# Kernel tuning notes

Measured on AMD Instinct MI355X. Metric: run time of the kernel, lower is better.

## Reference

```python
import jax, jax.numpy as jnp
import numpy as np

H = 16  # n_heads

def setup_inputs() -> dict:
    key = jax.random.key(0)
    ks = jax.random.split(key, 11)
    B, L, D = 2, 2048, 1024
    w = 1.0 / np.sqrt(D).astype(np.float32)
    return {
        "query": jax.random.normal(ks[0], (B, L, D), jnp.float32),
        "key":   jax.random.normal(ks[1], (B, L, D), jnp.float32),
        "value": jax.random.normal(ks[2], (B, L, D), jnp.float32),
        "Wq": jax.random.normal(ks[3], (D, D), jnp.float32) * w,
        "bq": jax.random.normal(ks[4], (D,), jnp.float32) * 0.01,
        "Wk": jax.random.normal(ks[5], (D, D), jnp.float32) * w,
        "bk": jax.random.normal(ks[6], (D,), jnp.float32) * 0.01,
        "Wv": jax.random.normal(ks[7], (D, D), jnp.float32) * w,
        "bv": jax.random.normal(ks[8], (D,), jnp.float32) * 0.01,
        "Wo": jax.random.normal(ks[9], (D, D), jnp.float32) * w,
        "bo": jax.random.normal(ks[10], (D,), jnp.float32) * 0.01,
        "masksize": 256,
    }

def reference(query, key, value, Wq, bq, Wk, bk, Wv, bv, Wo, bo, masksize):
    B, L, D = query.shape
    d_k = D // H
    scale = 1.0 / np.sqrt(d_k).astype(np.float32)

    def proj(x, W, b):
        # nn.Linear: x @ W.T + b, then [B,L,H,d_k] -> [B,H,L,d_k]
        return (x @ W.T + b).reshape(B, L, H, d_k).transpose(0, 2, 1, 3)

    q = proj(query, Wq, bq)
    k = proj(key, Wk, bk)
    v = proj(value, Wv, bv)

    # Sliding-window float mask (faithful to original: a 0/1 FLOAT tensor is
    # passed as attn_mask to SDPA, so it is ADDED to scores, not -inf-masked).
    half = masksize // 2
    i = jnp.arange(L)[:, None]
    j = jnp.arange(L)[None, :]
    band = (jnp.abs(i - j) <= half).astype(q.dtype)  # [L, L]

    scores = jnp.einsum('bhqd,bhkd->bhqk', q, k) * scale + band  # [B,H,L,L]
    attn = jax.nn.softmax(scores, axis=-1)
    out = jnp.einsum('bhqk,bhkd->bhqd', attn, v)  # [B,H,L,d_k]
    out = out.transpose(0, 2, 1, 3).reshape(B, L, D)
    return out @ Wo.T + bo
```

## Files before the change

### kernel.cpp

```cpp
#include <hip/hip_runtime.h>
#include <hip/hip_bf16.h>

#define Hh 16
#define Ll 2048
#define Dd 1024
#define DK 64
#define Mm 4096
#define Kk 1024
#define Nn 1024

typedef short bf16x8 __attribute__((ext_vector_type(8)));
typedef float f32x4 __attribute__((ext_vector_type(4)));

static __device__ __forceinline__ unsigned short f2bf(float f) {
    union { __hip_bfloat16 b; unsigned short u; } cv;
    cv.b = __float2bfloat16(f);
    return cv.u;
}

static __device__ __forceinline__ unsigned packtr(float a, float b) {
    return __builtin_amdgcn_perm(__builtin_bit_cast(unsigned, b),
                                 __builtin_bit_cast(unsigned, a), 0x07060302u);
}

static __device__ __forceinline__ float fexp2(float x) {
    return __builtin_amdgcn_exp2f(x);
}

static __device__ __forceinline__ void glds16(const ushort* g, ushort* l) {
    __builtin_amdgcn_global_load_lds((const __attribute__((address_space(1))) unsigned int*)g,
                                     (__attribute__((address_space(3))) unsigned int*)l,
                                     16, 0, 0);
}

__global__ __launch_bounds__(256) void cast_all(
    const float* __restrict__ q, const float* __restrict__ k, const float* __restrict__ v,
    const float* __restrict__ wq, const float* __restrict__ wk, const float* __restrict__ wv,
    const float* __restrict__ wo,
    ushort* __restrict__ qb, ushort* __restrict__ kb, ushort* __restrict__ vb,
    ushort* __restrict__ wqb, ushort* __restrict__ wkb, ushort* __restrict__ wvb,
    ushort* __restrict__ wob) {
    const int bx = blockIdx.x;
    const float4* s; ushort4* d; int base;
    if      (bx <  4096) { s = (const float4*)q;  d = (ushort4*)qb;  base = 0; }
    else if (bx <  8192) { s = (const float4*)k;  d = (ushort4*)kb;  base = 4096; }
    else if (bx < 12288) { s = (const float4*)v;  d = (ushort4*)vb;  base = 8192; }
    else if (bx < 13312) { s = (const float4*)wq; d = (ushort4*)wqb; base = 12288; }
    else if (bx < 14336) { s = (const float4*)wk; d = (ushort4*)wkb; base = 13312; }
    else if (bx < 15360) { s = (const float4*)wv; d = (ushort4*)wvb; base = 14336; }
    else                 { s = (const float4*)wo; d = (ushort4*)wob; base = 15360; }
    const int i = (bx - base) * 256 + threadIdx.x;
    float4 vv = s[i];
    ushort4 o;
    o.x = f2bf(vv.x); o.y = f2bf(vv.y); o.z = f2bf(vv.z); o.w = f2bf(vv.w);
    d[i] = o;
}

__global__ __launch_bounds__(256) void gemm_qkv(
    const ushort* __restrict__ A0, const ushort* __restrict__ A1, const ushort* __restrict__ A2,
    const ushort* __restrict__ W0, const ushort* __restrict__ W1, const ushort* __restrict__ W2,
    const float* __restrict__ b0, const float* __restrict__ b1, const float* __restrict__ b2,
    ushort* __restrict__ O0, ushort* __restrict__ O1, ushort* __restrict__ OVt) {
    __shared__ __align__(16) ushort SM[2 * 128 * 32];
    ushort* As = SM;
    ushort* Bs = SM + 4096;

    const int fl = blockIdx.x;
    const int xcd = fl & 7, bcoli = (fl >> 3) & 7, slot = fl >> 6;
    const int g = slot * 8 + xcd;
    const int z = g >> 5;
    const int browi = g & 31;

    const ushort* A = (z == 0) ? A0 : (z == 1) ? A1 : A2;
    const ushort* W = (z == 0) ? W0 : (z == 1) ? W1 : W2;
    const float* bias = (z == 0) ? b0 : (z == 1) ? b1 : b2;

    const int t = threadIdx.x;
    const int wave = t >> 6, lane = t & 63;
    const int quad = lane >> 4, l15 = lane & 15;
    const int brow = browi * 128, bcol = bcoli * 128;
    const int wr = (wave >> 1) * 64, wc = (wave & 1) * 64;
    const int gr = wave * 16 + (lane >> 2);
    const int gc = (lane & 3) * 8;

    f32x4 acc[4][4] = {};

    for (int k0 = 0; k0 < Kk; k0 += 32) {
        __syncthreads();
        glds16(A + (size_t)(brow + gr) * Kk + k0 + gc,      As + wave * 512);
        glds16(A + (size_t)(brow + 64 + gr) * Kk + k0 + gc, As + 2048 + wave * 512);
        glds16(W + (size_t)(bcol + gr) * Kk + k0 + gc,      Bs + wave * 512);
        glds16(W + (size_t)(bcol + 64 + gr) * Kk + k0 + gc, Bs + 2048 + wave * 512);
        __syncthreads();

        bf16x8 af[4], bfr[4];
#pragma unroll
        for (int i = 0; i < 4; i++)
            af[i] = *(const bf16x8*)(As + (wr + i * 16 + l15) * 32 + quad * 8);
#pragma unroll
        for (int j = 0; j < 4; j++)
            bfr[j] = *(const bf16x8*)(Bs + (wc + j * 16 + l15) * 32 + quad * 8);
#pragma unroll
        for (int i = 0; i < 4; i++)
#pragma unroll
            for (int j = 0; j < 4; j++)
                acc[i][j] = __builtin_amdgcn_mfma_f32_16x16x32_bf16(af[i], bfr[j], acc[i][j], 0, 0, 0);
    }

    if (z < 2) {
        ushort* Out = (z == 0) ? O0 : O1;
        const float oscl = (z == 0) ? 0.18033688f : 1.0f;
        const int b = brow >> 11;
        const int lbase = (brow & 2047) + wr;
        const int h = (bcol + wc) >> 6;
        ushort* T = SM + wave * 1280;
        __syncthreads();
#pragma unroll
        for (int i = 0; i < 4; i++) {
#pragma unroll
            for (int j = 0; j < 4; j++) {
                const float bv = bias[bcol + wc + j * 16 + l15];
#pragma unroll
                for (int r = 0; r < 4; r++)
                    T[(quad * 4 + r) * 80 + j * 16 + l15] = f2bf((acc[i][j][r] + bv) * oscl);
            }
            const int r8 = lane >> 3, c8 = lane & 7;
#pragma unroll
            for (int pass = 0; pass < 2; pass++) {
                const uint4 val = *(const uint4*)(T + (pass * 8 + r8) * 80 + c8 * 8);
                const int l = lbase + i * 16 + pass * 8 + r8;
                *(uint4*)(Out + ((size_t)(b * Hh + h) * Ll + l) * DK + c8 * 8) = val;
            }
        }
    } else {
        ushort* T = SM;
        const int b = brow >> 11;
        const int lbase = brow & 2047;
        const int npr = (wave & 1) * 16 + l15;
#pragma unroll
        for (int j = 0; j < 4; j++) {
            __syncthreads();
            const float bv = bias[bcol + wc + j * 16 + l15];
#pragma unroll
            for (int i = 0; i < 4; i++)
#pragma unroll
                for (int r = 0; r < 4; r++) {
                    const int m = wr + i * 16 + quad * 4 + r;
                    T[npr * 136 + m] = f2bf(acc[i][j][r] + bv);
                }
            __syncthreads();
#pragma unroll
            for (int cc = 0; cc < 2; cc++) {
                const int idx = t + cc * 256;
                const int ni = idx >> 4;
                const int ms = idx & 15;
                const int n = bcol + (ni >> 4) * 64 + j * 16 + (ni & 15);
                const int hh = n >> 6, dk = n & 63;
                uint4 val = *(const uint4*)(T + ni * 136 + ms * 8);
                *(uint4*)(OVt + ((size_t)(b * Hh + hh) * DK + dk) * Ll + lbase + ms * 8) = val;
            }
        }
    }
}

__global__ __launch_bounds__(256) void attn_kernel(const ushort* __restrict__ Q,
                                                   const ushort* __restrict__ Kp,
                                                   const ushort* __restrict__ Vt,
                                                   ushort* __restrict__ Oout,
                                                   const int* __restrict__ masksize) {
    __shared__ __align__(16) ushort Ks[2 * 128 * 32];
    __shared__ __align__(16) ushort Vs[64 * 128];
    const int t = threadIdx.x;
    const int wave = t >> 6, lane = t & 63;
    const int quad = lane >> 4, l15 = lane & 15;
    const int bx = blockIdx.x;
    const int bh = bx & 31, qc = bx >> 5;
    const int q0w = qc * 128 + wave * 32;
    const int half = masksize[0] >> 1;
    const unsigned wid = (unsigned)(2 * half);

    const ushort* Qb = Q + (size_t)bh * (Ll * DK);
    const ushort* Kb = Kp + (size_t)bh * (Ll * DK);
    const ushort* Vb = Vt + (size_t)bh * (DK * Ll);

    const bf16x8 qA0 = *(const bf16x8*)(Qb + (size_t)(q0w + l15) * DK + quad * 8);
    const bf16x8 qA1 = *(const bf16x8*)(Qb + (size_t)(q0w + l15) * DK + 32 + quad * 8);
    const bf16x8 qB0 = *(const bf16x8*)(Qb + (size_t)(q0w + 16 + l15) * DK + quad * 8);
    const bf16x8 qB1 = *(const bf16x8*)(Qb + (size_t)(q0w + 16 + l15) * DK + 32 + quad * 8);

    const float C2IN  = (1.0f - 24.0f) * 1.44269504088896f;
    const float C2OUT = -24.0f * 1.44269504088896f;
    const float E1 = 2.718281828f;

    bf16x8 onesf;
#pragma unroll
    for (int j = 0; j < 8; j++) onesf[j] = (short)0x3F80;

    f32x4 OA[4] = {}, OB[4] = {};
    f32x4 SA = {}, SB = {};

    const int krow = lane >> 2;
    const int kcol8 = (lane & 3) * 8;
    const int vdl = lane >> 4;
    const int vg0 = 2 * (lane & 15);

    for (int kt = 0; kt < Ll; kt += 128) {
        __syncthreads();
        if (wave < 2) {
            const int cbase = wave * 4;
#pragma unroll
            for (int c = 0; c < 4; c++)
#pragma unroll
                for (int pan = 0; pan < 2; pan++)
                    glds16(Kb + (size_t)(kt + (cbase + c) * 16 + krow) * DK + pan * 32 + kcol8,
                           Ks + (pan * 128 + (cbase + c) * 16) * 32);
        } else {
            const int sb = (wave - 2) * 8;
#pragma unroll
            for (int i = 0; i < 8; i++) {
                const int sidx = sb + i;
                const int d = sidx * 4 + vdl;
                const int g0 = vg0 ^ (d & 30);
                glds16(Vb + (size_t)d * Ll + kt + g0 * 4, Vs + sidx * 512);
            }
        }
        __syncthreads();

        const int qlo = q0w, qhi = q0w + 31;
        const bool allout = (kt + 127 < qlo - half) || (kt > qhi + half);
        const bool allin  = (kt >= qhi - half) && (kt + 127 <= qlo + half);
        const bool uniform = allin || allout;
        const float cinit = allin ? C2IN : C2OUT;
        f32x4 cvec = {cinit, cinit, cinit, cinit};

#pragma unroll
        for (int s = 0; s < 4; s++) {
            const bf16x8 kf00 = *(const bf16x8*)(Ks + ((2 * s) * 16 + l15) * 32 + quad * 8);
            const bf16x8 kf01 = *(const bf16x8*)(Ks + 4096 + ((2 * s) * 16 + l15) * 32 + quad * 8);
            const bf16x8 kf10 = *(const bf16x8*)(Ks + ((2 * s + 1) * 16 + l15) * 32 + quad * 8);
            const bf16x8 kf11 = *(const bf16x8*)(Ks + 4096 + ((2 * s + 1) * 16 + l15) * 32 + quad * 8);
            f32x4 zA0 = __builtin_amdgcn_mfma_f32_16x16x32_bf16(kf00, qA0, cvec, 0, 0, 0);
            zA0 = __builtin_amdgcn_mfma_f32_16x16x32_bf16(kf01, qA1, zA0, 0, 0, 0);
            f32x4 zA1 = __builtin_amdgcn_mfma_f32_16x16x32_bf16(kf10, qA0, cvec, 0, 0, 0);
            zA1 = __builtin_amdgcn_mfma_f32_16x16x32_bf16(kf11, qA1, zA1, 0, 0, 0);
            f32x4 zB0 = __builtin_amdgcn_mfma_f32_16x16x32_bf16(kf00, qB0, cvec, 0, 0, 0);
            zB0 = __builtin_amdgcn_mfma_f32_16x16x32_bf16(kf01, qB1, zB0, 0, 0, 0);
            f32x4 zB1 = __builtin_amdgcn_mfma_f32_16x16x32_bf16(kf10, qB0, cvec, 0, 0, 0);
            zB1 = __builtin_amdgcn_mfma_f32_16x16x32_bf16(kf11, qB1, zB1, 0, 0, 0);

            float pA[8], pB[8];
            if (uniform) {
#pragma unroll
                for (int g = 0; g < 2; g++)
#pragma unroll
                    for (int r = 0; r < 4; r++) {
                        pA[g * 4 + r] = fexp2(g ? zA1[r] : zA0[r]);
                        pB[g * 4 + r] = fexp2(g ? zB1[r] : zB0[r]);
                    }
            } else {
                const int kb = kt + s * 32 + quad * 4 + half;
#pragma unroll
                for (int g = 0; g < 2; g++)
#pragma unroll
                    for (int r = 0; r < 4; r++) {
                        const unsigned ttA = (unsigned)(kb + g * 16 + r - (q0w + l15));
                        const unsigned ttB = (unsigned)(kb + g * 16 + r - (q0w + 16 + l15));
                        pA[g * 4 + r] = fexp2(g ? zA1[r] : zA0[r]) * (ttA <= wid ? E1 : 1.0f);
                        pB[g * 4 + r] = fexp2(g ? zB1[r] : zB0[r]) * (ttB <= wid ? E1 : 1.0f);
                    }
            }

            bf16x8 pfA, pfB;
            ((unsigned*)&pfA)[0] = packtr(pA[0], pA[1]);
            ((unsigned*)&pfA)[1] = packtr(pA[2], pA[3]);
            ((unsigned*)&pfA)[2] = packtr(pA[4], pA[5]);
            ((unsigned*)&pfA)[3] = packtr(pA[6], pA[7]);
            ((unsigned*)&pfB)[0] = packtr(pB[0], pB[1]);
            ((unsigned*)&pfB)[1] = packtr(pB[2], pB[3]);
            ((unsigned*)&pfB)[2] = packtr(pB[4], pB[5]);
            ((unsigned*)&pfB)[3] = packtr(pB[6], pB[7]);

            SA = __builtin_amdgcn_mfma_f32_16x16x32_bf16(pfA, onesf, SA, 0, 0, 0);
            SB = __builtin_amdgcn_mfma_f32_16x16x32_bf16(pfB, onesf, SB, 0, 0, 0);

#pragma unroll
            for (int i = 0; i < 4; i++) {
                const int d = i * 16 + l15;
                const int x4 = (d & 30) * 4;
                const int bi = d * 128;
                const ushort4 v1 = *(const ushort4*)(Vs + bi + (((s * 8 + quad) * 4) ^ x4));
                const ushort4 v2 = *(const ushort4*)(Vs + bi + (((s * 8 + 4 + quad) * 4) ^ x4));
                bf16x8 vc;
                *(ushort4*)&vc = v1;
                *((ushort4*)&vc + 1) = v2;
                OA[i] = __builtin_amdgcn_mfma_f32_16x16x32_bf16(pfA, vc, OA[i], 0, 0, 0);
                OB[i] = __builtin_amdgcn_mfma_f32_16x16x32_bf16(pfB, vc, OB[i], 0, 0, 0);
            }
        }
    }

    float liA[4], liB[4];
#pragma unroll
    for (int r = 0; r < 4; r++) {
        liA[r] = 1.0f / SA[r];
        liB[r] = 1.0f / SB[r];
    }

    const int b = bh >> 4, h = bh & 15;
#pragma unroll
    for (int i = 0; i < 4; i++)
#pragma unroll
        for (int r = 0; r < 4; r++) {
            const int qa = q0w + quad * 4 + r;
            Oout[((size_t)b * Ll + qa) * Dd + h * DK + i * 16 + l15] = f2bf(OA[i][r] * liA[r]);
            Oout[((size_t)b * Ll + qa + 16) * Dd + h * DK + i * 16 + l15] = f2bf(OB[i][r] * liB[r]);
        }
}

__global__ __launch_bounds__(256) void gemm_o(const ushort* __restrict__ A,
                                              const ushort* __restrict__ W,
                                              const float* __restrict__ bias,
                                              float* __restrict__ Out) {
    __shared__ __align__(16) ushort As[64 * 32];
    __shared__ __align__(16) ushort Bs[128 * 32];
    const int fl = blockIdx.x;
    const int xcd = fl & 7, bcoli = (fl >> 3) & 7, slot = fl >> 6;
    const int g = slot * 8 + xcd;
    const int t = threadIdx.x;
    const int wave = t >> 6, lane = t & 63;
    const int quad = lane >> 4, l15 = lane & 15;
    const int brow = g * 64, bcol = bcoli * 128;
    const int wr = (wave >> 1) * 32, wc = (wave & 1) * 64;
    const int gr = wave * 16 + (lane >> 2);
    const int gc = (lane & 3) * 8;

    f32x4 acc[2][4] = {};

    for (int k0 = 0; k0 < Kk; k0 += 32) {
        __syncthreads();
        glds16(A + (size_t)(brow + gr) * Kk + k0 + gc,      As + wave * 512);
        glds16(W + (size_t)(bcol + gr) * Kk + k0 + gc,      Bs + wave * 512);
        glds16(W + (size_t)(bcol + 64 + gr) * Kk + k0 + gc, Bs + 2048 + wave * 512);
        __syncthreads();

        bf16x8 af[2], bfr[4];
#pragma unroll
        for (int i = 0; i < 2; i++)
            af[i] = *(const bf16x8*)(As + (wr + i * 16 + l15) * 32 + quad * 8);
#pragma unroll
        for (int j = 0; j < 4; j++)
            bfr[j] = *(const bf16x8*)(Bs + (wc + j * 16 + l15) * 32 + quad * 8);
#pragma unroll
        for (int i = 0; i < 2; i++)
#pragma unroll
            for (int j = 0; j < 4; j++)
                acc[i][j] = __builtin_amdgcn_mfma_f32_16x16x32_bf16(af[i], bfr[j], acc[i][j], 0, 0, 0);
    }

#pragma unroll
    for (int i = 0; i < 2; i++)
#pragma unroll
        for (int j = 0; j < 4; j++) {
            const int n = bcol + wc + j * 16 + l15;
            const float bv = bias[n];
#pragma unroll
            for (int r = 0; r < 4; r++) {
                const int m = brow + wr + i * 16 + quad * 4 + r;
                Out[(size_t)m * Nn + n] = acc[i][j][r] + bv;
            }
        }
}

extern "C" void kernel_launch(void* const* d_in, const int* in_sizes, int n_in,
                              void* d_out, int out_size, void* d_ws, size_t ws_size,
                              hipStream_t stream) {
    const float* query = (const float*)d_in[0];
    const float* key   = (const float*)d_in[1];
    const float* value = (const float*)d_in[2];
    const float* Wq = (const float*)d_in[3];
    const float* bq = (const float*)d_in[4];
    const float* Wk = (const float*)d_in[5];
    const float* bk = (const float*)d_in[6];
    const float* Wv = (const float*)d_in[7];
    const float* bv = (const float*)d_in[8];
    const float* Wo = (const float*)d_in[9];
    const float* bo = (const float*)d_in[10];
    const int* masksize = (const int*)d_in[11];

    char* ws = (char*)d_ws;
    const size_t MB = 1024 * 1024;
    ushort* qb  = (ushort*)(ws + 0 * MB);
    ushort* kbf = (ushort*)(ws + 8 * MB);
    ushort* vbf = (ushort*)(ws + 16 * MB);
    ushort* wqb = (ushort*)(ws + 24 * MB);
    ushort* wkb = (ushort*)(ws + 26 * MB);
    ushort* wvb = (ushort*)(ws + 28 * MB);
    ushort* wob = (ushort*)(ws + 30 * MB);
    ushort* Qp  = (ushort*)(ws + 32 * MB);
    ushort* Kp  = (ushort*)(ws + 40 * MB);
    ushort* Vt  = (ushort*)(ws + 48 * MB);
    ushort* AO  = (ushort*)(ws + 56 * MB);

    cast_all<<<16384, 256, 0, stream>>>(query, key, value, Wq, Wk, Wv, Wo,
                                        qb, kbf, vbf, wqb, wkb, wvb, wob);

    gemm_qkv<<<768, 256, 0, stream>>>(qb, kbf, vbf,
                                      wqb, wkb, wvb,
                                      bq, bk, bv,
                                      Qp, Kp, Vt);

    attn_kernel<<<512, 256, 0, stream>>>(Qp, Kp, Vt, AO, masksize);

    gemm_o<<<512, 256, 0, stream>>>(AO, wob, bo, (float*)d_out);
}
```

Baseline: 217.9 us.

## Split attention block into eight waves of sixteen query rows each

```diff
diff --git a/kernel.cpp b/kernel.cpp
--- a/kernel.cpp
+++ b/kernel.cpp
@@ -163,11 +163,11 @@
     }
 }
 
-__global__ __launch_bounds__(256) void attn_kernel(const ushort* __restrict__ Q,
-                                                   const ushort* __restrict__ Kp,
-                                                   const ushort* __restrict__ Vt,
-                                                   ushort* __restrict__ Oout,
-                                                   const int* __restrict__ masksize) {
+__global__ __launch_bounds__(512, 4) void attn_kernel(const ushort* __restrict__ Q,
+                                                      const ushort* __restrict__ Kp,
+                                                      const ushort* __restrict__ Vt,
+                                                      ushort* __restrict__ Oout,
+                                                      const int* __restrict__ masksize) {
     __shared__ __align__(16) ushort Ks[2 * 128 * 32];
     __shared__ __align__(16) ushort Vs[64 * 128];
     const int t = threadIdx.x;
@@ -175,7 +175,7 @@
     const int quad = lane >> 4, l15 = lane & 15;
     const int bx = blockIdx.x;
     const int bh = bx & 31, qc = bx >> 5;
-    const int q0w = qc * 128 + wave * 32;
+    const int q0w = qc * 128 + wave * 16;
     const int half = masksize[0] >> 1;
     const unsigned wid = (unsigned)(2 * half);
 
@@ -185,8 +185,6 @@
 
     const bf16x8 qA0 = *(const bf16x8*)(Qb + (size_t)(q0w + l15) * DK + quad * 8);
     const bf16x8 qA1 = *(const bf16x8*)(Qb + (size_t)(q0w + l15) * DK + 32 + quad * 8);
-    const bf16x8 qB0 = *(const bf16x8*)(Qb + (size_t)(q0w + 16 + l15) * DK + quad * 8);
-    const bf16x8 qB1 = *(const bf16x8*)(Qb + (size_t)(q0w + 16 + l15) * DK + 32 + quad * 8);
 
     const float C2IN  = (1.0f - 24.0f) * 1.44269504088896f;
     const float C2OUT = -24.0f * 1.44269504088896f;
@@ -196,8 +194,8 @@
 #pragma unroll
     for (int j = 0; j < 8; j++) onesf[j] = (short)0x3F80;
 
-    f32x4 OA[4] = {}, OB[4] = {};
-    f32x4 SA = {}, SB = {};
+    f32x4 OA[4] = {};
+    f32x4 SA = {};
 
     const int krow = lane >> 2;
     const int kcol8 = (lane & 3) * 8;
@@ -206,18 +204,18 @@
 
     for (int kt = 0; kt < Ll; kt += 128) {
         __syncthreads();
-        if (wave < 2) {
-            const int cbase = wave * 4;
-#pragma unroll
-            for (int c = 0; c < 4; c++)
+        if (wave < 4) {
+            const int cbase = wave * 2;
+#pragma unroll
+            for (int c = 0; c < 2; c++)
 #pragma unroll
                 for (int pan = 0; pan < 2; pan++)
                     glds16(Kb + (size_t)(kt + (cbase + c) * 16 + krow) * DK + pan * 32 + kcol8,
                            Ks + (pan * 128 + (cbase + c) * 16) * 32);
         } else {
-            const int sb = (wave - 2) * 8;
-#pragma unroll
-            for (int i = 0; i < 8; i++) {
+            const int sb = (wave - 4) * 4;
+#pragma unroll
+            for (int i = 0; i < 4; i++) {
                 const int sidx = sb + i;
                 const int d = sidx * 4 + vdl;
                 const int g0 = vg0 ^ (d & 30);
@@ -226,7 +224,7 @@
         }
         __syncthreads();
 
-        const int qlo = q0w, qhi = q0w + 31;
+        const int qlo = q0w, qhi = q0w + 15;
         const bool allout = (kt + 127 < qlo - half) || (kt > qhi + half);
         const bool allin  = (kt >= qhi - half) && (kt + 127 <= qlo + half);
         const bool uniform = allin || allout;
@@ -243,20 +241,14 @@
             zA0 = __builtin_amdgcn_mfma_f32_16x16x32_bf16(kf01, qA1, zA0, 0, 0, 0);
             f32x4 zA1 = __builtin_amdgcn_mfma_f32_16x16x32_bf16(kf10, qA0, cvec, 0, 0, 0);
             zA1 = __builtin_amdgcn_mfma_f32_16x16x32_bf16(kf11, qA1, zA1, 0, 0, 0);
-            f32x4 zB0 = __builtin_amdgcn_mfma_f32_16x16x32_bf16(kf00, qB0, cvec, 0, 0, 0);
-            zB0 = __builtin_amdgcn_mfma_f32_16x16x32_bf16(kf01, qB1, zB0, 0, 0, 0);
-            f32x4 zB1 = __builtin_amdgcn_mfma_f32_16x16x32_bf16(kf10, qB0, cvec, 0, 0, 0);
-            zB1 = __builtin_amdgcn_mfma_f32_16x16x32_bf16(kf11, qB1, zB1, 0, 0, 0);
-
-            float pA[8], pB[8];
+
+            float pA[8];
             if (uniform) {
 #pragma unroll
                 for (int g = 0; g < 2; g++)
 #pragma unroll
-                    for (int r = 0; r < 4; r++) {
+                    for (int r = 0; r < 4; r++)
                         pA[g * 4 + r] = fexp2(g ? zA1[r] : zA0[r]);
-                        pB[g * 4 + r] = fexp2(g ? zB1[r] : zB0[r]);
-                    }
             } else {
                 const int kb = kt + s * 32 + quad * 4 + half;
 #pragma unroll
@@ -264,24 +256,17 @@
 #pragma unroll
                     for (int r = 0; r < 4; r++) {
                         const unsigned ttA = (unsigned)(kb + g * 16 + r - (q0w + l15));
-                        const unsigned ttB = (unsigned)(kb + g * 16 + r - (q0w + 16 + l15));
                         pA[g * 4 + r] = fexp2(g ? zA1[r] : zA0[r]) * (ttA <= wid ? E1 : 1.0f);
-                        pB[g * 4 + r] = fexp2(g ? zB1[r] : zB0[r]) * (ttB <= wid ? E1 : 1.0f);
                     }
             }
 
-            bf16x8 pfA, pfB;
+            bf16x8 pfA;
             ((unsigned*)&pfA)[0] = packtr(pA[0], pA[1]);
             ((unsigned*)&pfA)[1] = packtr(pA[2], pA[3]);
             ((unsigned*)&pfA)[2] = packtr(pA[4], pA[5]);
             ((unsigned*)&pfA)[3] = packtr(pA[6], pA[7]);
-            ((unsigned*)&pfB)[0] = packtr(pB[0], pB[1]);
-            ((unsigned*)&pfB)[1] = packtr(pB[2], pB[3]);
-            ((unsigned*)&pfB)[2] = packtr(pB[4], pB[5]);
-            ((unsigned*)&pfB)[3] = packtr(pB[6], pB[7]);
 
             SA = __builtin_amdgcn_mfma_f32_16x16x32_bf16(pfA, onesf, SA, 0, 0, 0);
-            SB = __builtin_amdgcn_mfma_f32_16x16x32_bf16(pfB, onesf, SB, 0, 0, 0);
 
 #pragma unroll
             for (int i = 0; i < 4; i++) {
@@ -294,17 +279,13 @@
                 *(ushort4*)&vc = v1;
                 *((ushort4*)&vc + 1) = v2;
                 OA[i] = __builtin_amdgcn_mfma_f32_16x16x32_bf16(pfA, vc, OA[i], 0, 0, 0);
-                OB[i] = __builtin_amdgcn_mfma_f32_16x16x32_bf16(pfB, vc, OB[i], 0, 0, 0);
             }
         }
     }
 
-    float liA[4], liB[4];
-#pragma unroll
-    for (int r = 0; r < 4; r++) {
-        liA[r] = 1.0f / SA[r];
-        liB[r] = 1.0f / SB[r];
-    }
+    float liA[4];
+#pragma unroll
+    for (int r = 0; r < 4; r++) liA[r] = 1.0f / SA[r];
 
     const int b = bh >> 4, h = bh & 15;
 #pragma unroll
@@ -313,7 +294,6 @@
         for (int r = 0; r < 4; r++) {
             const int qa = q0w + quad * 4 + r;
             Oout[((size_t)b * Ll + qa) * Dd + h * DK + i * 16 + l15] = f2bf(OA[i][r] * liA[r]);
-            Oout[((size_t)b * Ll + qa + 16) * Dd + h * DK + i * 16 + l15] = f2bf(OB[i][r] * liB[r]);
         }
 }
 
@@ -409,7 +389,7 @@
                                       bq, bk, bv,
                                       Qp, Kp, Vt);
 
-    attn_kernel<<<512, 256, 0, stream>>>(Qp, Kp, Vt, AO, masksize);
+    attn_kernel<<<512, 512, 0, stream>>>(Qp, Kp, Vt, AO, masksize);
 
     gemm_o<<<512, 256, 0, stream>>>(AO, wob, bo, (float*)d_out);
 }
```

After: 220.5 us. About the same (+1.2%).

## Split attention key range across two wave groups and swizzle K LDS layout

Applied to the files above, without the earlier changes.

```diff
diff --git a/kernel.cpp b/kernel.cpp
--- a/kernel.cpp
+++ b/kernel.cpp
@@ -163,21 +163,24 @@
     }
 }
 
-__global__ __launch_bounds__(256) void attn_kernel(const ushort* __restrict__ Q,
-                                                   const ushort* __restrict__ Kp,
-                                                   const ushort* __restrict__ Vt,
-                                                   ushort* __restrict__ Oout,
-                                                   const int* __restrict__ masksize) {
-    __shared__ __align__(16) ushort Ks[2 * 128 * 32];
-    __shared__ __align__(16) ushort Vs[64 * 128];
+__global__ __launch_bounds__(512, 4) void attn_kernel(const ushort* __restrict__ Q,
+                                                      const ushort* __restrict__ Kp,
+                                                      const ushort* __restrict__ Vt,
+                                                      ushort* __restrict__ Oout,
+                                                      const int* __restrict__ masksize) {
+    __shared__ __align__(16) ushort SM[4 * 8192];
     const int t = threadIdx.x;
     const int wave = t >> 6, lane = t & 63;
     const int quad = lane >> 4, l15 = lane & 15;
     const int bx = blockIdx.x;
     const int bh = bx & 31, qc = bx >> 5;
-    const int q0w = qc * 128 + wave * 32;
+    const int p = wave & 3, h = wave >> 2;
+    const int q0w = qc * 128 + p * 32;
     const int half = masksize[0] >> 1;
     const unsigned wid = (unsigned)(2 * half);
+
+    ushort* KsH = SM + h * 8192;
+    ushort* VsH = SM + 16384 + h * 8192;
 
     const ushort* Qb = Q + (size_t)bh * (Ll * DK);
     const ushort* Kb = Kp + (size_t)bh * (Ll * DK);
@@ -200,28 +203,32 @@
     f32x4 SA = {}, SB = {};
 
     const int krow = lane >> 2;
-    const int kcol8 = (lane & 3) * 8;
+    const int kcol8 = (((lane & 3) ^ ((lane >> 3) & 3)) * 8);
+    const int qsw8 = (quad ^ ((l15 >> 1) & 3)) * 8;
     const int vdl = lane >> 4;
     const int vg0 = 2 * (lane & 15);
 
-    for (int kt = 0; kt < Ll; kt += 128) {
-        __syncthreads();
-        if (wave < 2) {
-            const int cbase = wave * 4;
-#pragma unroll
-            for (int c = 0; c < 4; c++)
+    for (int it = 0; it < 8; ++it) {
+        const int kt = h * 1024 + it * 128;
+        __syncthreads();
+        if ((wave & 2) == 0) {
+            const int a = wave & 1;
+#pragma unroll
+            for (int c = 0; c < 4; c++) {
+                const int cidx = a * 4 + c;
 #pragma unroll
                 for (int pan = 0; pan < 2; pan++)
-                    glds16(Kb + (size_t)(kt + (cbase + c) * 16 + krow) * DK + pan * 32 + kcol8,
-                           Ks + (pan * 128 + (cbase + c) * 16) * 32);
+                    glds16(Kb + (size_t)(kt + cidx * 16 + krow) * DK + pan * 32 + kcol8,
+                           KsH + (pan * 128 + cidx * 16) * 32);
+            }
         } else {
-            const int sb = (wave - 2) * 8;
+            const int a = wave & 1;
 #pragma unroll
             for (int i = 0; i < 8; i++) {
-                const int sidx = sb + i;
+                const int sidx = a * 8 + i;
                 const int d = sidx * 4 + vdl;
                 const int g0 = vg0 ^ (d & 30);
-                glds16(Vb + (size_t)d * Ll + kt + g0 * 4, Vs + sidx * 512);
+                glds16(Vb + (size_t)d * Ll + kt + g0 * 4, VsH + sidx * 512);
             }
         }
         __syncthreads();
@@ -235,10 +242,10 @@
 
 #pragma unroll
         for (int s = 0; s < 4; s++) {
-            const bf16x8 kf00 = *(const bf16x8*)(Ks + ((2 * s) * 16 + l15) * 32 + quad * 8);
-            const bf16x8 kf01 = *(const bf16x8*)(Ks + 4096 + ((2 * s) * 16 + l15) * 32 + quad * 8);
-            const bf16x8 kf10 = *(const bf16x8*)(Ks + ((2 * s + 1) * 16 + l15) * 32 + quad * 8);
-            const bf16x8 kf11 = *(const bf16x8*)(Ks + 4096 + ((2 * s + 1) * 16 + l15) * 32 + quad * 8);
+            const bf16x8 kf00 = *(const bf16x8*)(KsH + ((2 * s) * 16 + l15) * 32 + qsw8);
+            const bf16x8 kf01 = *(const bf16x8*)(KsH + 4096 + ((2 * s) * 16 + l15) * 32 + qsw8);
+            const bf16x8 kf10 = *(const bf16x8*)(KsH + ((2 * s + 1) * 16 + l15) * 32 + qsw8);
+            const bf16x8 kf11 = *(const bf16x8*)(KsH + 4096 + ((2 * s + 1) * 16 + l15) * 32 + qsw8);
             f32x4 zA0 = __builtin_amdgcn_mfma_f32_16x16x32_bf16(kf00, qA0, cvec, 0, 0, 0);
             zA0 = __builtin_amdgcn_mfma_f32_16x16x32_bf16(kf01, qA1, zA0, 0, 0, 0);
             f32x4 zA1 = __builtin_amdgcn_mfma_f32_16x16x32_bf16(kf10, qA0, cvec, 0, 0, 0);
@@ -288,8 +295,8 @@
                 const int d = i * 16 + l15;
                 const int x4 = (d & 30) * 4;
                 const int bi = d * 128;
-                const ushort4 v1 = *(const ushort4*)(Vs + bi + (((s * 8 + quad) * 4) ^ x4));
-                const ushort4 v2 = *(const ushort4*)(Vs + bi + (((s * 8 + 4 + quad) * 4) ^ x4));
+                const ushort4 v1 = *(const ushort4*)(VsH + bi + (((s * 8 + quad) * 4) ^ x4));
+                const ushort4 v2 = *(const ushort4*)(VsH + bi + (((s * 8 + 4 + quad) * 4) ^ x4));
                 bf16x8 vc;
                 *(ushort4*)&vc = v1;
                 *((ushort4*)&vc + 1) = v2;
@@ -299,22 +306,49 @@
         }
     }
 
-    float liA[4], liB[4];
-#pragma unroll
-    for (int r = 0; r < 4; r++) {
-        liA[r] = 1.0f / SA[r];
-        liB[r] = 1.0f / SB[r];
-    }
-
-    const int b = bh >> 4, h = bh & 15;
-#pragma unroll
-    for (int i = 0; i < 4; i++)
+    float* LC = (float*)SM;
+    const int col = p * 64 + lane;
+    __syncthreads();
+    if (h == 1) {
+#pragma unroll
+        for (int i = 0; i < 4; i++)
+#pragma unroll
+            for (int r = 0; r < 4; r++) {
+                LC[(i * 4 + r) * 256 + col] = OA[i][r];
+                LC[(16 + i * 4 + r) * 256 + col] = OB[i][r];
+            }
 #pragma unroll
         for (int r = 0; r < 4; r++) {
-            const int qa = q0w + quad * 4 + r;
-            Oout[((size_t)b * Ll + qa) * Dd + h * DK + i * 16 + l15] = f2bf(OA[i][r] * liA[r]);
-            Oout[((size_t)b * Ll + qa + 16) * Dd + h * DK + i * 16 + l15] = f2bf(OB[i][r] * liB[r]);
-        }
+            LC[(32 + r) * 256 + col] = SA[r];
+            LC[(36 + r) * 256 + col] = SB[r];
+        }
+    }
+    __syncthreads();
+    if (h == 0) {
+#pragma unroll
+        for (int i = 0; i < 4; i++)
+#pragma unroll
+            for (int r = 0; r < 4; r++) {
+                OA[i][r] += LC[(i * 4 + r) * 256 + col];
+                OB[i][r] += LC[(16 + i * 4 + r) * 256 + col];
+            }
+        float liA[4], liB[4];
+#pragma unroll
+        for (int r = 0; r < 4; r++) {
+            liA[r] = 1.0f / (SA[r] + LC[(32 + r) * 256 + col]);
+            liB[r] = 1.0f / (SB[r] + LC[(36 + r) * 256 + col]);
+        }
+
+        const int b = bh >> 4, hh = bh & 15;
+#pragma unroll
+        for (int i = 0; i < 4; i++)
+#pragma unroll
+            for (int r = 0; r < 4; r++) {
+                const int qa = q0w + quad * 4 + r;
+                Oout[((size_t)b * Ll + qa) * Dd + hh * DK + i * 16 + l15] = f2bf(OA[i][r] * liA[r]);
+                Oout[((size_t)b * Ll + qa + 16) * Dd + hh * DK + i * 16 + l15] = f2bf(OB[i][r] * liB[r]);
+            }
+    }
 }
 
 __global__ __launch_bounds__(256) void gemm_o(const ushort* __restrict__ A,
@@ -409,7 +443,7 @@
                                       bq, bk, bv,
                                       Qp, Kp, Vt);
 
-    attn_kernel<<<512, 256, 0, stream>>>(Qp, Kp, Vt, AO, masksize);
+    attn_kernel<<<512, 512, 0, stream>>>(Qp, Kp, Vt, AO, masksize);
 
     gemm_o<<<512, 256, 0, stream>>>(AO, wob, bo, (float*)d_out);
 }
```

Result: slower. 363.3 us (+66.8%).

## Double-buffer K/V tiles in LDS and swizzle K layout in attention

Applied to the files above, without the earlier changes.

```diff
diff --git a/kernel.cpp b/kernel.cpp
--- a/kernel.cpp
+++ b/kernel.cpp
@@ -168,8 +168,7 @@
                                                    const ushort* __restrict__ Vt,
                                                    ushort* __restrict__ Oout,
                                                    const int* __restrict__ masksize) {
-    __shared__ __align__(16) ushort Ks[2 * 128 * 32];
-    __shared__ __align__(16) ushort Vs[64 * 128];
+    __shared__ __align__(16) ushort SM[32768];
     const int t = threadIdx.x;
     const int wave = t >> 6, lane = t & 63;
     const int quad = lane >> 4, l15 = lane & 15;
@@ -200,31 +199,46 @@
     f32x4 SA = {}, SB = {};
 
     const int krow = lane >> 2;
-    const int kcol8 = (lane & 3) * 8;
+    const int kcol8 = (((lane & 3) ^ ((lane >> 3) & 3)) * 8);
+    const int qsw8 = (quad ^ ((l15 >> 1) & 3)) * 8;
     const int vdl = lane >> 4;
     const int vg0 = 2 * (lane & 15);
 
-    for (int kt = 0; kt < Ll; kt += 128) {
-        __syncthreads();
-        if (wave < 2) {
-            const int cbase = wave * 4;
-#pragma unroll
-            for (int c = 0; c < 4; c++)
-#pragma unroll
-                for (int pan = 0; pan < 2; pan++)
-                    glds16(Kb + (size_t)(kt + (cbase + c) * 16 + krow) * DK + pan * 32 + kcol8,
-                           Ks + (pan * 128 + (cbase + c) * 16) * 32);
-        } else {
-            const int sb = (wave - 2) * 8;
-#pragma unroll
-            for (int i = 0; i < 8; i++) {
-                const int sidx = sb + i;
-                const int d = sidx * 4 + vdl;
-                const int g0 = vg0 ^ (d & 30);
-                glds16(Vb + (size_t)d * Ll + kt + g0 * 4, Vs + sidx * 512);
-            }
-        }
-        __syncthreads();
+#define STAGE_KV(KT, BUF)                                                                  \
+    do {                                                                                   \
+        ushort* Ksb_ = SM + (BUF) * 8192;                                                  \
+        ushort* Vsb_ = SM + 16384 + (BUF) * 8192;                                          \
+        if (wave < 2) {                                                                    \
+            const int cbase_ = wave * 4;                                                   \
+            _Pragma("unroll")                                                              \
+            for (int c_ = 0; c_ < 4; c_++)                                                 \
+                _Pragma("unroll")                                                          \
+                for (int pan_ = 0; pan_ < 2; pan_++)                                       \
+                    glds16(Kb + (size_t)((KT) + (cbase_ + c_) * 16 + krow) * DK            \
+                               + pan_ * 32 + kcol8,                                        \
+                           Ksb_ + (pan_ * 128 + (cbase_ + c_) * 16) * 32);                 \
+        } else {                                                                           \
+            const int sb_ = (wave - 2) * 8;                                                \
+            _Pragma("unroll")                                                              \
+            for (int i_ = 0; i_ < 8; i_++) {                                               \
+                const int sidx_ = sb_ + i_;                                                \
+                const int d_ = sidx_ * 4 + vdl;                                            \
+                const int g0_ = vg0 ^ (d_ & 30);                                           \
+                glds16(Vb + (size_t)d_ * Ll + (KT) + g0_ * 4, Vsb_ + sidx_ * 512);         \
+            }                                                                              \
+        }                                                                                  \
+    } while (0)
+
+    STAGE_KV(0, 0);
+    int cur = 0;
+
+    for (int it = 0; it < 16; ++it) {
+        const int kt = it * 128;
+        __syncthreads();
+        if (it < 15) STAGE_KV(kt + 128, cur ^ 1);
+
+        const ushort* Ksb = SM + cur * 8192;
+        const ushort* Vsb = SM + 16384 + cur * 8192;
 
         const int qlo = q0w, qhi = q0w + 31;
         const bool allout = (kt + 127 < qlo - half) || (kt > qhi + half);
@@ -235,10 +249,10 @@
 
 #pragma unroll
         for (int s = 0; s < 4; s++) {
-            const bf16x8 kf00 = *(const bf16x8*)(Ks + ((2 * s) * 16 + l15) * 32 + quad * 8);
-            const bf16x8 kf01 = *(const bf16x8*)(Ks + 4096 + ((2 * s) * 16 + l15) * 32 + quad * 8);
-            const bf16x8 kf10 = *(const bf16x8*)(Ks + ((2 * s + 1) * 16 + l15) * 32 + quad * 8);
-            const bf16x8 kf11 = *(const bf16x8*)(Ks + 4096 + ((2 * s + 1) * 16 + l15) * 32 + quad * 8);
+            const bf16x8 kf00 = *(const bf16x8*)(Ksb + ((2 * s) * 16 + l15) * 32 + qsw8);
+            const bf16x8 kf01 = *(const bf16x8*)(Ksb + 4096 + ((2 * s) * 16 + l15) * 32 + qsw8);
+            const bf16x8 kf10 = *(const bf16x8*)(Ksb + ((2 * s + 1) * 16 + l15) * 32 + qsw8);
+            const bf16x8 kf11 = *(const bf16x8*)(Ksb + 4096 + ((2 * s + 1) * 16 + l15) * 32 + qsw8);
             f32x4 zA0 = __builtin_amdgcn_mfma_f32_16x16x32_bf16(kf00, qA0, cvec, 0, 0, 0);
             zA0 = __builtin_amdgcn_mfma_f32_16x16x32_bf16(kf01, qA1, zA0, 0, 0, 0);
             f32x4 zA1 = __builtin_amdgcn_mfma_f32_16x16x32_bf16(kf10, qA0, cvec, 0, 0, 0);
@@ -288,8 +302,8 @@
                 const int d = i * 16 + l15;
                 const int x4 = (d & 30) * 4;
                 const int bi = d * 128;
-                const ushort4 v1 = *(const ushort4*)(Vs + bi + (((s * 8 + quad) * 4) ^ x4));
-                const ushort4 v2 = *(const ushort4*)(Vs + bi + (((s * 8 + 4 + quad) * 4) ^ x4));
+                const ushort4 v1 = *(const ushort4*)(Vsb + bi + (((s * 8 + quad) * 4) ^ x4));
+                const ushort4 v2 = *(const ushort4*)(Vsb + bi + (((s * 8 + 4 + quad) * 4) ^ x4));
                 bf16x8 vc;
                 *(ushort4*)&vc = v1;
                 *((ushort4*)&vc + 1) = v2;
@@ -297,7 +311,9 @@
                 OB[i] = __builtin_amdgcn_mfma_f32_16x16x32_bf16(pfB, vc, OB[i], 0, 0, 0);
             }
         }
+        cur ^= 1;
     }
+#undef STAGE_KV
 
     float liA[4], liB[4];
 #pragma unroll
```

New measurement: 218.5 us. Within noise of the previous version (+0.3%).
